# Performance work log

Hardware: AMD Instinct MI355X
Metric: run time of the kernel (lower is better)

Reference implementation:

```python
import jax, jax.numpy as jnp
import numpy as np

B, S, HID, MEM, NW = 32, 256, 1024, 256, 1024
PLAST, IMP = 0.1, 1.0
W_SCALE = 0.02  # sane init for projection weights


def setup_inputs() -> dict:
    key = jax.random.key(0)
    ks = jax.random.split(key, 24)
    n = lambda k, sh, s=1.0: jax.random.normal(k, sh, dtype=jnp.float32) * s
    inp = {
        "q": n(ks[0], (B, S, HID)),
        "data": n(ks[1], (NW, HID)),
        "episodic_k": n(ks[2], (MEM, HID)),
        "episodic_v": n(ks[3], (MEM, HID)),
        "semantic_k": n(ks[4], (MEM, HID)),
        "semantic_v": n(ks[5], (MEM, HID)),
        "working_m": n(ks[6], (1, 10, HID)),
    }
    i = 7
    for name in ("atte", "atts", "attw"):
        inp[name + "_in_w"] = n(ks[i], (3 * HID, HID), W_SCALE); i += 1
        inp[name + "_in_b"] = jnp.zeros((3 * HID,), jnp.float32)
        inp[name + "_out_w"] = n(ks[i], (HID, HID), W_SCALE); i += 1
        inp[name + "_out_b"] = jnp.zeros((HID,), jnp.float32)
    inp["proj_w"] = n(ks[i], (HID, 3 * HID), W_SCALE)
    inp["proj_b"] = jnp.zeros((HID,), jnp.float32)
    return inp


def mha_shared_kv(q, k, v, in_w, in_b, out_w, out_b, n_heads):
    # q: [B,S,H]; k,v: [M,H] (memory bank shared across the batch)
    d = q.shape[-1] // n_heads
    wq, wk, wv = jnp.split(in_w, 3, axis=0)
    bq, bk, bv = jnp.split(in_b, 3)
    Bq, Sq, _ = q.shape
    M = k.shape[0]
    qh = (q @ wq.T + bq).reshape(Bq, Sq, n_heads, d)   # [B,S,h,d]
    kh = (k @ wk.T + bk).reshape(M, n_heads, d)        # [M,h,d]
    vh = (v @ wv.T + bv).reshape(M, n_heads, d)
    scale = 1.0 / jnp.sqrt(jnp.float32(d))
    att = jax.nn.softmax(jnp.einsum('bshd,mhd->bhsm', qh, kh) * scale, axis=-1)
    o = jnp.einsum('bhsm,mhd->bshd', att, vh).reshape(Bq, Sq, -1)
    return o @ out_w.T + out_b


def reference(q, data, episodic_k, episodic_v, semantic_k, semantic_v, working_m,
              atte_in_w, atte_in_b, atte_out_w, atte_out_b,
              atts_in_w, atts_in_b, atts_out_w, atts_out_b,
              attw_in_w, attw_in_b, attw_out_w, attw_out_b,
              proj_w, proj_b):
    # ---- write(data, 'episodic'): softmax-addressed fast-weight update ----
    probs = jax.nn.softmax(data @ episodic_k.T, axis=-1)          # [N,M]
    w = probs * (PLAST * IMP)                                     # [N,M]
    u = w.mean(axis=0)[:, None]                                   # [M,1] mean update strength per slot
    writes = jnp.einsum('nm,nh->mh', w, data) / NW                # mean_n data[n]*w[n,m]
    ek = jax.lax.stop_gradient(episodic_k * (1.0 - u) + writes)   # .data assignment -> no grad
    ev = jax.lax.stop_gradient(episodic_v * (1.0 - u) + writes)
    # ---- read(q): 3 small attentions over memory banks, concat, project ----
    e_r = mha_shared_kv(q, ek, ev, atte_in_w, atte_in_b, atte_out_w, atte_out_b, 16)
    s_r = mha_shared_kv(q, semantic_k, semantic_v, atts_in_w, atts_in_b, atts_out_w, atts_out_b, 16)
    w_r = mha_shared_kv(q, working_m[0], working_m[0], attw_in_w, attw_in_b, attw_out_w, attw_out_b, 8)
    cat = jnp.concatenate((e_r, s_r, w_r), axis=-1)               # [B,S,3H]
    return cat @ proj_w.T + proj_b                                # [B,S,H]
```

## Files before the change

### kernel.cpp

```cpp
#include <hip/hip_runtime.h>
#include <hip/hip_bf16.h>


using bf = __hip_bfloat16;
using short8v = __attribute__((ext_vector_type(8))) short;
using f32x4  = __attribute__((ext_vector_type(4))) float;

#define GLOAD_LDS16(g, l) __builtin_amdgcn_global_load_lds( \
    (const __attribute__((address_space(1))) void*)(g), \
    (__attribute__((address_space(3))) void*)(l), 16, 0, 0)

__device__ inline float bf2f(unsigned short s) {
    union { unsigned u; float f; } c; c.u = ((unsigned)s) << 16; return c.f;
}
__device__ inline unsigned short f2bu(float x) {
    union { float f; unsigned u; } c; c.f = x;
    unsigned r = c.u + 0x7FFF + ((c.u >> 16) & 1);
    return (unsigned short)(r >> 16);
}
__device__ inline void storeC(float* p, float v) { *p = v; }
__device__ inline void storeC(bf* p, float v) { *p = __float2bfloat16(v); }

template <bool AF32>
__global__ __launch_bounds__(256) void gemm_bt(
    const void* __restrict__ Av, int lda,
    const bf* __restrict__ B, int ldb,
    float* __restrict__ part, int M, int N, int K)
{
    __shared__ short As[128 * 64];
    __shared__ short Bs[128 * 64];
    const int nbn = N >> 7;
    const int bm = blockIdx.x / nbn, bn = blockIdx.x % nbn;
    const int t = threadIdx.x;
    const int w = t >> 6, lane = t & 63;
    const int wr = w >> 1, wc = w & 1;
    const int l16 = lane & 15, lhi = lane >> 4;
    const int kc = K / gridDim.y;
    const int kbeg = blockIdx.y * kc, kend = kbeg + kc;

    f32x4 acc[4][4];
    #pragma unroll
    for (int i = 0; i < 4; ++i)
        #pragma unroll
        for (int j = 0; j < 4; ++j) { f32x4 z = {0.f, 0.f, 0.f, 0.f}; acc[i][j] = z; }

    const bf*    Arow  = (const bf*)Av + (size_t)bm * 128 * lda;
    const float* Afrow = (const float*)Av + (size_t)bm * 128 * lda;
    const bf*    Brow  = B + (size_t)bn * 128 * ldb;

    for (int k0 = kbeg; k0 < kend; k0 += 64) {
        #pragma unroll
        for (int j = 0; j < 4; ++j) {
            int u = (w * 4 + j) * 64 + lane;
            int row = u >> 3, c8 = u & 7;
            int slot = c8 ^ (row & 7);
            GLOAD_LDS16(Brow + (size_t)row * ldb + k0 + slot * 8, &Bs[(w * 4 + j) * 512]);
            if (!AF32)
                GLOAD_LDS16(Arow + (size_t)row * lda + k0 + slot * 8, &As[(w * 4 + j) * 512]);
        }
        if (AF32) {
            #pragma unroll
            for (int r = 0; r < 4; ++r) {
                int u = t + (r << 8);
                int row = u >> 3, c8 = u & 7;
                const float* src = Afrow + (size_t)row * lda + k0 + c8 * 8;
                float4 v0 = *(const float4*)src;
                float4 v1 = *(const float4*)(src + 4);
                short8v sv;
                sv[0] = (short)f2bu(v0.x); sv[1] = (short)f2bu(v0.y);
                sv[2] = (short)f2bu(v0.z); sv[3] = (short)f2bu(v0.w);
                sv[4] = (short)f2bu(v1.x); sv[5] = (short)f2bu(v1.y);
                sv[6] = (short)f2bu(v1.z); sv[7] = (short)f2bu(v1.w);
                *(short8v*)&As[row * 64 + ((c8 ^ (row & 7)) * 8)] = sv;
            }
        }
        __syncthreads();
        #pragma unroll
        for (int kk = 0; kk < 2; ++kk) {
            short8v af[4], bfr[4];
            #pragma unroll
            for (int mt = 0; mt < 4; ++mt) {
                int row = wr * 64 + mt * 16 + l16;
                int slot = (kk * 4 + lhi) ^ (row & 7);
                af[mt] = *(const short8v*)&As[row * 64 + slot * 8];
            }
            #pragma unroll
            for (int nt = 0; nt < 4; ++nt) {
                int row = wc * 64 + nt * 16 + l16;
                int slot = (kk * 4 + lhi) ^ (row & 7);
                bfr[nt] = *(const short8v*)&Bs[row * 64 + slot * 8];
            }
            #pragma unroll
            for (int mt = 0; mt < 4; ++mt)
                #pragma unroll
                for (int nt = 0; nt < 4; ++nt)
                    acc[mt][nt] = __builtin_amdgcn_mfma_f32_16x16x32_bf16(
                        af[mt], bfr[nt], acc[mt][nt], 0, 0, 0);
        }
        __syncthreads();
    }
    #pragma unroll
    for (int mt = 0; mt < 4; ++mt)
        #pragma unroll
        for (int nt = 0; nt < 4; ++nt) {
            int col = bn * 128 + wc * 64 + nt * 16 + l16;
            #pragma unroll
            for (int j = 0; j < 4; ++j) {
                int rowg = bm * 128 + wr * 64 + mt * 16 + lhi * 4 + j;
                part[(size_t)blockIdx.y * M * N + (size_t)rowg * N + col] = acc[mt][nt][j];
            }
        }
}

template <typename CT, bool AF32, bool XSWZ>
__global__ __launch_bounds__(512) void gemm256(
    const void* __restrict__ Av, int lda,
    const bf* __restrict__ B, int ldb,
    const float* __restrict__ bias,
    CT* __restrict__ C, int ldc,
    int M, int N, int K)
{
    __shared__ short As[256 * 64];
    __shared__ short Bs[128 * 64];
    const int nbn = N >> 7;
    int bid = blockIdx.x;
    if (XSWZ) bid = (bid & 7) * (gridDim.x >> 3) + (bid >> 3);
    const int bm = bid / nbn, bn = bid % nbn;
    const int t = threadIdx.x;
    const int w = t >> 6, lane = t & 63;
    const int wr = w >> 1, wc = w & 1;
    const int l16 = lane & 15, lhi = lane >> 4;

    f32x4 acc[4][4];
    #pragma unroll
    for (int i = 0; i < 4; ++i)
        #pragma unroll
        for (int j = 0; j < 4; ++j) { f32x4 z = {0.f, 0.f, 0.f, 0.f}; acc[i][j] = z; }

    const bf*    Arow  = (const bf*)Av + (size_t)bm * 256 * lda;
    const float* Afrow = (const float*)Av + (size_t)bm * 256 * lda;
    const bf*    Brow  = B + (size_t)bn * 128 * ldb;

    for (int k0 = 0; k0 < K; k0 += 64) {
        #pragma unroll
        for (int j = 0; j < 2; ++j) {
            int u = t + (j << 9);
            int row = u >> 3, c8 = u & 7;
            int slot = c8 ^ (row & 7);
            GLOAD_LDS16(Brow + (size_t)row * ldb + k0 + slot * 8, &Bs[(j * 8 + w) * 512]);
        }
        if (!AF32) {
            #pragma unroll
            for (int j = 0; j < 4; ++j) {
                int u = t + (j << 9);
                int row = u >> 3, c8 = u & 7;
                int slot = c8 ^ (row & 7);
                GLOAD_LDS16(Arow + (size_t)row * lda + k0 + slot * 8, &As[(j * 8 + w) * 512]);
            }
        } else {
            #pragma unroll
            for (int r = 0; r < 4; ++r) {
                int u = t + (r << 9);
                int row = u >> 3, c8 = u & 7;
                const float* src = Afrow + (size_t)row * lda + k0 + c8 * 8;
                float4 v0 = *(const float4*)src;
                float4 v1 = *(const float4*)(src + 4);
                short8v sv;
                sv[0] = (short)f2bu(v0.x); sv[1] = (short)f2bu(v0.y);
                sv[2] = (short)f2bu(v0.z); sv[3] = (short)f2bu(v0.w);
                sv[4] = (short)f2bu(v1.x); sv[5] = (short)f2bu(v1.y);
                sv[6] = (short)f2bu(v1.z); sv[7] = (short)f2bu(v1.w);
                *(short8v*)&As[row * 64 + ((c8 ^ (row & 7)) * 8)] = sv;
            }
        }
        __syncthreads();
        #pragma unroll
        for (int kk = 0; kk < 2; ++kk) {
            short8v af[4], bfr[4];
            #pragma unroll
            for (int mt = 0; mt < 4; ++mt) {
                int row = wr * 64 + mt * 16 + l16;
                int slot = (kk * 4 + lhi) ^ (row & 7);
                af[mt] = *(const short8v*)&As[row * 64 + slot * 8];
            }
            #pragma unroll
            for (int nt = 0; nt < 4; ++nt) {
                int row = wc * 64 + nt * 16 + l16;
                int slot = (kk * 4 + lhi) ^ (row & 7);
                bfr[nt] = *(const short8v*)&Bs[row * 64 + slot * 8];
            }
            #pragma unroll
            for (int mt = 0; mt < 4; ++mt)
                #pragma unroll
                for (int nt = 0; nt < 4; ++nt)
                    acc[mt][nt] = __builtin_amdgcn_mfma_f32_16x16x32_bf16(
                        af[mt], bfr[nt], acc[mt][nt], 0, 0, 0);
        }
        __syncthreads();
    }
    #pragma unroll
    for (int mt = 0; mt < 4; ++mt)
        #pragma unroll
        for (int nt = 0; nt < 4; ++nt) {
            int col = bn * 128 + wc * 64 + nt * 16 + l16;
            float bv = bias ? bias[col] : 0.0f;
            #pragma unroll
            for (int j = 0; j < 4; ++j) {
                int rowg = bm * 256 + wr * 64 + mt * 16 + lhi * 4 + j;
                storeC(&C[(size_t)rowg * ldc + col], acc[mt][nt][j] + bv);
            }
        }
}

struct GG { const float* A; const bf* B; const float* bias; bf* out;
            int lda, ldb, M, N, ldo, xoff; };
struct GG7 { GG g[7]; };

__global__ __launch_bounds__(256) void ggemm(GG7 P)
{
    __shared__ short As[128 * 64];
    __shared__ short Bs[128 * 64];
    const int bid = blockIdx.x;
    int gidx = 0;
    #pragma unroll
    for (int i = 1; i < 7; ++i) if (bid >= P.g[i].xoff) gidx = i;
    const GG d = P.g[gidx];
    const int lb = bid - d.xoff;
    const int nbn = d.N >> 7;
    const int bm = lb / nbn, bn = lb % nbn;
    const int t = threadIdx.x;
    const int w = t >> 6, lane = t & 63;
    const int wr = w >> 1, wc = w & 1;
    const int l16 = lane & 15, lhi = lane >> 4;

    f32x4 acc[4][4];
    #pragma unroll
    for (int i = 0; i < 4; ++i)
        #pragma unroll
        for (int j = 0; j < 4; ++j) { f32x4 z = {0.f, 0.f, 0.f, 0.f}; acc[i][j] = z; }

    const float* Afrow = d.A + (size_t)bm * 128 * d.lda;
    const bf*    Brow  = d.B + (size_t)bn * 128 * d.ldb;

    for (int k0 = 0; k0 < 1024; k0 += 64) {
        #pragma unroll
        for (int j = 0; j < 4; ++j) {
            int u = (w * 4 + j) * 64 + lane;
            int row = u >> 3, c8 = u & 7;
            int slot = c8 ^ (row & 7);
            GLOAD_LDS16(Brow + (size_t)row * d.ldb + k0 + slot * 8, &Bs[(w * 4 + j) * 512]);
        }
        #pragma unroll
        for (int r = 0; r < 4; ++r) {
            int u = t + (r << 8);
            int row = u >> 3, c8 = u & 7;
            const float* src = Afrow + (size_t)row * d.lda + k0 + c8 * 8;
            float4 v0 = *(const float4*)src;
            float4 v1 = *(const float4*)(src + 4);
            short8v sv;
            sv[0] = (short)f2bu(v0.x); sv[1] = (short)f2bu(v0.y);
            sv[2] = (short)f2bu(v0.z); sv[3] = (short)f2bu(v0.w);
            sv[4] = (short)f2bu(v1.x); sv[5] = (short)f2bu(v1.y);
            sv[6] = (short)f2bu(v1.z); sv[7] = (short)f2bu(v1.w);
            *(short8v*)&As[row * 64 + ((c8 ^ (row & 7)) * 8)] = sv;
        }
        __syncthreads();
        #pragma unroll
        for (int kk = 0; kk < 2; ++kk) {
            short8v af[4], bfr[4];
            #pragma unroll
            for (int mt = 0; mt < 4; ++mt) {
                int row = wr * 64 + mt * 16 + l16;
                int slot = (kk * 4 + lhi) ^ (row & 7);
                af[mt] = *(const short8v*)&As[row * 64 + slot * 8];
            }
            #pragma unroll
            for (int nt = 0; nt < 4; ++nt) {
                int row = wc * 64 + nt * 16 + l16;
                int slot = (kk * 4 + lhi) ^ (row & 7);
                bfr[nt] = *(const short8v*)&Bs[row * 64 + slot * 8];
            }
            #pragma unroll
            for (int mt = 0; mt < 4; ++mt)
                #pragma unroll
                for (int nt = 0; nt < 4; ++nt)
                    acc[mt][nt] = __builtin_amdgcn_mfma_f32_16x16x32_bf16(
                        af[mt], bfr[nt], acc[mt][nt], 0, 0, 0);
        }
        __syncthreads();
    }
    #pragma unroll
    for (int mt = 0; mt < 4; ++mt)
        #pragma unroll
        for (int nt = 0; nt < 4; ++nt) {
            int col = bn * 128 + wc * 64 + nt * 16 + l16;
            float bv = d.bias ? d.bias[col] : 0.0f;
            #pragma unroll
            for (int j = 0; j < 4; ++j) {
                int rowg = bm * 128 + wr * 64 + mt * 16 + lhi * 4 + j;
                d.out[(size_t)rowg * d.ldo + col]
                    = __float2bfloat16(acc[mt][nt][j] + bv);
            }
        }
}

__global__ __launch_bounds__(512) void attn_es(
    bf* Ocat, const bf* __restrict__ khE, const bf* __restrict__ khS,
    const bf* __restrict__ vTE, const bf* __restrict__ vTS)
{
    __shared__ short Ks[256 * 64];
    __shared__ short Vs[64 * 256];
    const int bank = blockIdx.x >> 10;
    const int lbid = blockIdx.x & 1023;
    const bf* kh  = bank ? khS : khE;
    const bf* vhT = bank ? vTS : vTE;
    bf* QO = Ocat + bank * 1024;
    const int qt = lbid >> 4, head = lbid & 15;
    const int t = threadIdx.x, w = t >> 6, lane = t & 63;
    const int l16 = lane & 15, lhi = lane >> 4;
    const float scale = 0.125f;

    #pragma unroll
    for (int j = 0; j < 4; ++j) {
        int ublk = w * 4 + j;
        int u = ublk * 64 + lane;
        { int row = u >> 3, c8 = u & 7;
          int slot = c8 ^ (row & 7);
          GLOAD_LDS16(kh + (size_t)row * 1024 + head * 64 + slot * 8, &Ks[ublk * 512]); }
        { int row = u >> 5, c16 = u & 31;
          int slot = c16 ^ (row & 7);
          GLOAD_LDS16(vhT + (size_t)(head * 64 + row) * 256 + slot * 8, &Vs[ublk * 512]); }
    }
    const int qr = qt * 128 + w * 16 + l16;
    short8v aq0 = *(const short8v*)(QO + (size_t)qr * 3072 + head * 64 + lhi * 8);
    short8v aq1 = *(const short8v*)(QO + (size_t)qr * 3072 + head * 64 + 32 + lhi * 8);
    __syncthreads();

    f32x4 sc[16];
    #pragma unroll
    for (int nt = 0; nt < 16; ++nt) { f32x4 z = {0.f, 0.f, 0.f, 0.f}; sc[nt] = z; }
    #pragma unroll
    for (int nt = 0; nt < 16; ++nt) {
        int row = nt * 16 + l16;
        #pragma unroll
        for (int kk = 0; kk < 2; ++kk) {
            int slot = (kk * 4 + lhi) ^ (row & 7);
            short8v b = *(const short8v*)&Ks[row * 64 + slot * 8];
            sc[nt] = __builtin_amdgcn_mfma_f32_16x16x32_bf16(kk ? aq1 : aq0, b, sc[nt], 0, 0, 0);
        }
    }
    float inv[4];
    #pragma unroll
    for (int j = 0; j < 4; ++j) {
        float m_ = -1e30f;
        #pragma unroll
        for (int nt = 0; nt < 16; ++nt) m_ = fmaxf(m_, sc[nt][j]);
        #pragma unroll
        for (int off = 8; off; off >>= 1) m_ = fmaxf(m_, __shfl_xor(m_, off));
        float s_ = 0.f;
        #pragma unroll
        for (int nt = 0; nt < 16; ++nt) {
            float e = __expf((sc[nt][j] - m_) * scale);
            sc[nt][j] = e; s_ += e;
        }
        #pragma unroll
        for (int off = 8; off; off >>= 1) s_ += __shfl_xor(s_, off);
        inv[j] = 1.0f / s_;
    }
    __syncthreads();

    char* Pw = (char*)Ks + w * 4096;
    f32x4 oa[4];
    #pragma unroll
    for (int nt = 0; nt < 4; ++nt) { f32x4 z = {0.f, 0.f, 0.f, 0.f}; oa[nt] = z; }
    #pragma unroll
    for (int h = 0; h < 2; ++h) {
        #pragma unroll
        for (int nt = 0; nt < 8; ++nt) {
            int colL = nt * 16 + l16;
            #pragma unroll
            for (int j = 0; j < 4; ++j) {
                int row = lhi * 4 + j;
                *(short*)(Pw + row * 256 + ((colL * 2) ^ ((row & 7) << 4)))
                    = (short)f2bu(sc[h * 8 + nt][j] * inv[j]);
            }
        }
        #pragma unroll
        for (int kk = 0; kk < 4; ++kk) {
            short8v a = *(const short8v*)(Pw + l16 * 256 + (((kk * 32 + lhi * 8) * 2) ^ ((l16 & 7) << 4)));
            #pragma unroll
            for (int nt = 0; nt < 4; ++nt) {
                int row = nt * 16 + l16;
                int m = h * 128 + kk * 32 + lhi * 8;
                short8v b = *(const short8v*)((const char*)Vs + row * 512 + ((m * 2) ^ ((row & 7) << 4)));
                oa[nt] = __builtin_amdgcn_mfma_f32_16x16x32_bf16(a, b, oa[nt], 0, 0, 0);
            }
        }
    }
    #pragma unroll
    for (int nt = 0; nt < 4; ++nt)
        #pragma unroll
        for (int j = 0; j < 4; ++j)
            QO[(size_t)(qt * 128 + w * 16 + lhi * 4 + j) * 3072 + head * 64 + nt * 16 + l16]
                = __float2bfloat16(oa[nt][j]);
}

__global__ __launch_bounds__(256) void attn_w(
    bf* QOp, const bf* __restrict__ khw, const bf* __restrict__ vhw)
{
    const int bs = blockIdx.x;
    const int t = threadIdx.x;
    const int head = t >> 5;
    const int dg = head * 128 + (t & 31) * 4;

    ushort4 qv = *(const ushort4*)(QOp + (size_t)bs * 3072 + dg);
    float q0 = bf2f(qv.x), q1 = bf2f(qv.y), q2 = bf2f(qv.z), q3 = bf2f(qv.w);
    float s[10];
    #pragma unroll
    for (int m = 0; m < 10; ++m) {
        ushort4 kv = *(const ushort4*)(khw + (size_t)m * 1024 + dg);
        float pr = q0 * bf2f(kv.x) + q1 * bf2f(kv.y) + q2 * bf2f(kv.z) + q3 * bf2f(kv.w);
        #pragma unroll
        for (int off = 16; off; off >>= 1) pr += __shfl_xor(pr, off);
        s[m] = pr * 0.08838834764831845f;
    }
    float mx = s[0];
    #pragma unroll
    for (int m = 1; m < 10; ++m) mx = fmaxf(mx, s[m]);
    float pp[10], sum = 0.f;
    #pragma unroll
    for (int m = 0; m < 10; ++m) { pp[m] = __expf(s[m] - mx); sum += pp[m]; }
    float inv = 1.0f / sum;
    float o0 = 0, o1 = 0, o2 = 0, o3 = 0;
    #pragma unroll
    for (int m = 0; m < 10; ++m) {
        ushort4 vv = *(const ushort4*)(vhw + (size_t)m * 1024 + dg);
        o0 += pp[m] * bf2f(vv.x); o1 += pp[m] * bf2f(vv.y);
        o2 += pp[m] * bf2f(vv.z); o3 += pp[m] * bf2f(vv.w);
    }
    bf* op = QOp + (size_t)bs * 3072 + dg;
    op[0] = __float2bfloat16(o0 * inv); op[1] = __float2bfloat16(o1 * inv);
    op[2] = __float2bfloat16(o2 * inv); op[3] = __float2bfloat16(o3 * inv);
}

struct CS { const float* src; bf* dst; int voff; };
struct MP {
    CS cs[8];
    const float* tsrc[4]; bf* tdst[4];
    const float* ow[3]; const float* ob[3]; const float* ib[3];
    float* bp;
    const float* inb_e; const float* inb_s; float* bqcat3;
    const float* wm; const float* inw_w; const float* inb_w;
    bf* khw; bf* vhw;
};

__global__ __launch_bounds__(256) void megaprep(MP P)
{
    __shared__ unsigned short tile[64][65];
    const int bid = blockIdx.x;
    const int t = threadIdx.x;
    if (bid < 13824) {
        int gi = bid * 256 + t;
        int gidx = 0;
        #pragma unroll
        for (int i = 1; i < 8; ++i) if (gi >= P.cs[i].voff) gidx = i;
        int i = (gi - P.cs[gidx].voff) * 4;
        float4 v = *(const float4*)(P.cs[gidx].src + i);
        ushort4 o;
        o.x = f2bu(v.x); o.y = f2bu(v.y); o.z = f2bu(v.z); o.w = f2bu(v.w);
        *(ushort4*)((unsigned short*)P.cs[gidx].dst + i) = o;
    } else if (bid < 14848) {
        int lb = bid - 13824;
        int sel = lb >> 8, bb = lb & 255;
        const float* in = P.tsrc[sel];
        bf* outT = P.tdst[sel];
        int bx = bb & 15, by = bb >> 4;
        int r0 = by * 64, c0 = bx * 64;
        int tr = t >> 4, tc4 = (t & 15) * 4;
        #pragma unroll
        for (int i = 0; i < 4; ++i) {
            int r = tr + i * 16;
            float4 v = *(const float4*)(in + (size_t)(r0 + r) * 1024 + c0 + tc4);
            tile[r][tc4 + 0] = f2bu(v.x); tile[r][tc4 + 1] = f2bu(v.y);
            tile[r][tc4 + 2] = f2bu(v.z); tile[r][tc4 + 3] = f2bu(v.w);
        }
        __syncthreads();
        #pragma unroll
        for (int i = 0; i < 4; ++i) {
            int r = tr + i * 16;
            ushort4 v;
            v.x = tile[tc4 + 0][r]; v.y = tile[tc4 + 1][r];
            v.z = tile[tc4 + 2][r]; v.w = tile[tc4 + 3][r];
            *(ushort4*)((unsigned short*)outT + (size_t)(c0 + r) * 1024 + r0 + tc4) = v;
        }
    } else if (bid < 15616) {
        int g = (bid - 14848) * 4 + (t >> 6);
        int lane = t & 63;
        int bank = g >> 10, j = g & 1023;
        const float* ow = P.ow[bank];
        const float* xx = P.ib[bank] + 2048;
        const float* wrow = ow + (size_t)j * 1024;
        float acc = 0.f;
        #pragma unroll
        for (int cc = 0; cc < 4; ++cc) {
            float4 a = *(const float4*)(wrow + lane * 16 + cc * 4);
            float4 x = *(const float4*)(xx + lane * 16 + cc * 4);
            acc += a.x * x.x + a.y * x.y + a.z * x.z + a.w * x.w;
        }
        #pragma unroll
        for (int off = 32; off; off >>= 1) acc += __shfl_xor(acc, off);
        if (lane == 0) P.bp[g] = acc + P.ob[bank][j];
    } else if (bid < 15628) {
        int i = (bid - 15616) * 256 + t;
        if (i < 1024) P.bqcat3[i] = P.inb_e[i];
        else if (i < 2048) P.bqcat3[i] = P.inb_s[i - 1024];
        else P.bqcat3[i] = P.inb_w[i - 2048];
    } else {
        int o = (bid - 15628) * 4 + (t >> 6);
        int lane = t & 63;
        int sel = o >= 10240;
        int o2 = o - sel * 10240;
        int m = o2 >> 10, c = o2 & 1023;
        const float* wrow = P.inw_w + (size_t)(1024 + sel * 1024 + c) * 1024;
        const float* xrow = P.wm + (size_t)m * 1024;
        float acc = 0.f;
        #pragma unroll
        for (int cc = 0; cc < 4; ++cc) {
            float4 a = *(const float4*)(wrow + lane * 16 + cc * 4);
            float4 x = *(const float4*)(xrow + lane * 16 + cc * 4);
            acc += a.x * x.x + a.y * x.y + a.z * x.z + a.w * x.w;
        }
        #pragma unroll
        for (int off = 32; off; off >>= 1) acc += __shfl_xor(acc, off);
        if (lane == 0) {
            float v = acc + (sel ? 0.f : P.inb_w[1024 + c]);
            (sel ? P.vhw : P.khw)[(size_t)m * 1024 + c] = __float2bfloat16(v);
        }
    }
}


__global__ __launch_bounds__(256) void btot_kern(
    const float* __restrict__ bp, const float* __restrict__ pw,
    const float* __restrict__ pb, float* __restrict__ btot)
{
    int j = blockIdx.x * 4 + (threadIdx.x >> 6);
    int lane = threadIdx.x & 63;
    const float* row = pw + (size_t)j * 3072;
    float acc = 0.f;
    #pragma unroll
    for (int it = 0; it < 12; ++it) {
        int c = lane * 4 + it * 256;
        float4 a = *(const float4*)(row + c);
        float4 x = *(const float4*)(bp + c);
        acc += a.x * x.x + a.y * x.y + a.z * x.z + a.w * x.w;
    }
    #pragma unroll
    for (int off = 32; off; off >>= 1) acc += __shfl_xor(acc, off);
    if (lane == 0) btot[j] = acc + pb[j];
}

__global__ __launch_bounds__(256) void write_softmax_p(const float* __restrict__ part,
                                                       bf* __restrict__ wT)
{
    const int n = blockIdx.x, m = threadIdx.x;
    float s = 0.f;
    #pragma unroll
    for (int k = 0; k < 8; ++k) s += part[(size_t)k * 262144 + n * 256 + m];
    float mx = s;
    #pragma unroll
    for (int off = 32; off; off >>= 1) mx = fmaxf(mx, __shfl_xor(mx, off));
    __shared__ float red[4], red2[4];
    int w = threadIdx.x >> 6;
    if ((threadIdx.x & 63) == 0) red[w] = mx;
    __syncthreads();
    mx = fmaxf(fmaxf(red[0], red[1]), fmaxf(red[2], red[3]));
    float e = __expf(s - mx);
    float sm = e;
    #pragma unroll
    for (int off = 32; off; off >>= 1) sm += __shfl_xor(sm, off);
    if ((threadIdx.x & 63) == 0) red2[w] = sm;
    __syncthreads();
    sm = red2[0] + red2[1] + red2[2] + red2[3];
    wT[(size_t)m * 1024 + n] = __float2bfloat16(0.1f * e / sm);
}

__global__ __launch_bounds__(256) void usum_kern(const bf* __restrict__ wT, float* __restrict__ u)
{
    int w = threadIdx.x >> 6, lane = threadIdx.x & 63;
    int m = blockIdx.x * 4 + w;
    const bf* row = wT + (size_t)m * 1024;
    float s = 0.f;
    for (int i = lane; i < 1024; i += 64) s += __bfloat162float(row[i]);
    #pragma unroll
    for (int off = 32; off; off >>= 1) s += __shfl_xor(s, off);
    if (lane == 0) u[m] = s * (1.0f / 1024.0f);
}

__global__ __launch_bounds__(256) void update_fused(
    const float* __restrict__ epk, const float* __restrict__ epv,
    const float* __restrict__ u, const float* __restrict__ part,
    float* __restrict__ ekf, bf* __restrict__ evb)
{
    int i = blockIdx.x * 256 + threadIdx.x;
    int m = i >> 10;
    float wr = 0.f;
    #pragma unroll
    for (int k = 0; k < 8; ++k) wr += part[(size_t)k * 262144 + i];
    wr *= (1.0f / 1024.0f);
    float f = 1.0f - u[m];
    ekf[i] = epk[i] * f + wr;
    evb[i] = __float2bfloat16(epv[i] * f + wr);
}

extern "C" void kernel_launch(void* const* d_in, const int* in_sizes, int n_in,
                              void* d_out, int out_size, void* d_ws, size_t ws_size,
                              hipStream_t stream)
{
    const float* q     = (const float*)d_in[0];
    const float* data  = (const float*)d_in[1];
    const float* epk   = (const float*)d_in[2];
    const float* epv   = (const float*)d_in[3];
    const float* smk   = (const float*)d_in[4];
    const float* smv   = (const float*)d_in[5];
    const float* wm    = (const float*)d_in[6];
    const float* inw_e = (const float*)d_in[7];  const float* inb_e = (const float*)d_in[8];
    const float* ow_e  = (const float*)d_in[9];  const float* ob_e  = (const float*)d_in[10];
    const float* inw_s = (const float*)d_in[11]; const float* inb_s = (const float*)d_in[12];
    const float* ow_s  = (const float*)d_in[13]; const float* ob_s  = (const float*)d_in[14];
    const float* inw_w = (const float*)d_in[15]; const float* inb_w = (const float*)d_in[16];
    const float* ow_w  = (const float*)d_in[17]; const float* ob_w  = (const float*)d_in[18];
    const float* pw    = (const float*)d_in[19]; const float* pb    = (const float*)d_in[20];
    float* out  = (float*)d_out;
    float* part = (float*)d_out;
    bf* qb = (bf*)((char*)d_out + 8388608);

    char* p = (char*)d_ws;
    auto alloc = [&](size_t bytes) -> char* {
        char* r = p; p += (bytes + 255) & ~(size_t)255; return r;
    };
    float* u      = (float*)alloc(256 * 4);
    float* bp     = (float*)alloc(3072 * 4);
    float* btot   = (float*)alloc(1024 * 4);
    float* bqcat3 = (float*)alloc(3072 * 4);
    float* ekf    = (float*)alloc((size_t)256 * 1024 * 4);
    bf* wT     = (bf*)alloc(256 * 1024 * 2);
    bf* dT     = (bf*)alloc((size_t)1024 * 1024 * 2);
    bf* epkb   = (bf*)alloc(256 * 1024 * 2);
    bf* smvb   = (bf*)alloc(256 * 1024 * 2);
    bf* evb    = (bf*)alloc(256 * 1024 * 2);
    bf* khE    = (bf*)alloc(256 * 1024 * 2);
    bf* khS    = (bf*)alloc(256 * 1024 * 2);
    bf* vTE    = (bf*)alloc((size_t)1024 * 256 * 2);
    bf* vTS    = (bf*)alloc((size_t)1024 * 256 * 2);
    bf* khw    = (bf*)alloc(10 * 1024 * 2);
    bf* vhw    = (bf*)alloc(10 * 1024 * 2);
    bf* Wall   = (bf*)alloc((size_t)3072 * 1024 * 2);
    bf* WkE    = (bf*)alloc((size_t)1024 * 1024 * 2);
    bf* WkS    = (bf*)alloc((size_t)1024 * 1024 * 2);
    bf* owT0   = (bf*)alloc((size_t)1024 * 1024 * 2);
    bf* owT1   = (bf*)alloc((size_t)1024 * 1024 * 2);
    bf* owT2   = (bf*)alloc((size_t)1024 * 1024 * 2);
    bf* Gcat   = (bf*)alloc((size_t)1024 * 3072 * 2);
    bf* Ocat   = (bf*)alloc((size_t)8192 * 3072 * 2);
    if ((size_t)(p - (char*)d_ws) > ws_size) return;

    {
        MP P;
        CS cs[8] = { {q, qb, 0},
                     {epk, epkb, 2097152}, {smv, smvb, 2162688},
                     {inw_e, Wall, 2228224},
                     {inw_s, Wall + (size_t)1024 * 1024, 2490368},
                     {inw_w, Wall + (size_t)2048 * 1024, 2752512},
                     {inw_e + (size_t)1024 * 1024, WkE, 3014656},
                     {inw_s + (size_t)1024 * 1024, WkS, 3276800} };
        for (int i = 0; i < 8; ++i) P.cs[i] = cs[i];
        P.tsrc[0] = data; P.tdst[0] = dT;
        P.tsrc[1] = ow_e; P.tdst[1] = owT0;
        P.tsrc[2] = ow_s; P.tdst[2] = owT1;
        P.tsrc[3] = ow_w; P.tdst[3] = owT2;
        P.ow[0] = ow_e; P.ow[1] = ow_s; P.ow[2] = ow_w;
        P.ob[0] = ob_e; P.ob[1] = ob_s; P.ob[2] = ob_w;
        P.ib[0] = inb_e; P.ib[1] = inb_s; P.ib[2] = inb_w;
        P.bp = bp;
        P.inb_e = inb_e; P.inb_s = inb_s; P.bqcat3 = bqcat3;
        P.wm = wm; P.inw_w = inw_w; P.inb_w = inb_w;
        P.khw = khw; P.vhw = vhw;
        megaprep<<<20748, 256, 0, stream>>>(P);
    }
    btot_kern<<<256, 256, 0, stream>>>(bp, pw, pb, btot);

    gemm_bt<true><<<dim3(16, 8), 256, 0, stream>>>(data, 1024, epkb, 1024, part, 1024, 256, 1024);
    write_softmax_p<<<1024, 256, 0, stream>>>(part, wT);
    usum_kern<<<64, 256, 0, stream>>>(wT, u);
    gemm_bt<false><<<dim3(16, 8), 256, 0, stream>>>(wT, 1024, dT, 1024, part, 256, 1024, 1024);
    update_fused<<<1024, 256, 0, stream>>>(epk, epv, u, part, ekf, evb);

    gemm256<bf, false, true><<<768, 512, 0, stream>>>(
        qb, 1024, Wall, 1024, bqcat3, Ocat, 3072, 8192, 3072, 1024);

    {
        GG7 G = {{
            { ekf,                         WkE,  inb_e + 1024, khE,         1024, 1024,  256, 1024, 1024, 0   },
            { smk,                         WkS,  inb_s + 1024, khS,         1024, 1024,  256, 1024, 1024, 16  },
            { inw_e + (size_t)2048 * 1024, evb,  nullptr,      vTE,         1024, 1024, 1024,  256,  256, 32  },
            { inw_s + (size_t)2048 * 1024, smvb, nullptr,      vTS,         1024, 1024, 1024,  256,  256, 48  },
            { pw + 0,                      owT0, nullptr,      Gcat + 0,    3072, 1024, 1024, 1024, 3072, 64  },
            { pw + 1024,                   owT1, nullptr,      Gcat + 1024, 3072, 1024, 1024, 1024, 3072, 128 },
            { pw + 2048,                   owT2, nullptr,      Gcat + 2048, 3072, 1024, 1024, 1024, 3072, 192 },
        }};
        ggemm<<<256, 256, 0, stream>>>(G);
    }

    attn_es<<<2048, 512, 0, stream>>>(Ocat, khE, khS, vTE, vTS);
    attn_w<<<8192, 256, 0, stream>>>(Ocat + 2048, khw, vhw);

    gemm256<float, false, true><<<256, 512, 0, stream>>>(
        Ocat, 3072, Gcat, 3072, btot, out, 1024, 8192, 1024, 3072);
}
```

Before: 299.7 us.

## Pre-convert fp32 GEMM operands to bf16 and double-buffer the final projection GEMM

Moves the fp32-to-bf16 conversion of data, proj_w, semantic_k and the V input weights into the megaprep pass. The GEMM kernels can then load A tiles straight into LDS with async global-to-LDS loads instead of converting in registers. The episodic key update now writes bf16 directly. The final output GEMM switches to a new double-buffered kernel that overlaps the next K-tile load with MFMA compute. The cost is larger megaprep work, extra workspace, and a scratch bf16 proj_w copy placed in the output buffer.

```diff
diff --git a/kernel.cpp b/kernel.cpp
--- a/kernel.cpp
+++ b/kernel.cpp
@@ -21,9 +21,8 @@
 __device__ inline void storeC(float* p, float v) { *p = v; }
 __device__ inline void storeC(bf* p, float v) { *p = __float2bfloat16(v); }
 
-template <bool AF32>
 __global__ __launch_bounds__(256) void gemm_bt(
-    const void* __restrict__ Av, int lda,
+    const bf* __restrict__ A, int lda,
     const bf* __restrict__ B, int ldb,
     float* __restrict__ part, int M, int N, int K)
 {
@@ -44,9 +43,8 @@
         #pragma unroll
         for (int j = 0; j < 4; ++j) { f32x4 z = {0.f, 0.f, 0.f, 0.f}; acc[i][j] = z; }
 
-    const bf*    Arow  = (const bf*)Av + (size_t)bm * 128 * lda;
-    const float* Afrow = (const float*)Av + (size_t)bm * 128 * lda;
-    const bf*    Brow  = B + (size_t)bn * 128 * ldb;
+    const bf* Arow = A + (size_t)bm * 128 * lda;
+    const bf* Brow = B + (size_t)bn * 128 * ldb;
 
     for (int k0 = kbeg; k0 < kend; k0 += 64) {
         #pragma unroll
@@ -55,24 +53,7 @@
             int row = u >> 3, c8 = u & 7;
             int slot = c8 ^ (row & 7);
             GLOAD_LDS16(Brow + (size_t)row * ldb + k0 + slot * 8, &Bs[(w * 4 + j) * 512]);
-            if (!AF32)
-                GLOAD_LDS16(Arow + (size_t)row * lda + k0 + slot * 8, &As[(w * 4 + j) * 512]);
-        }
-        if (AF32) {
-            #pragma unroll
-            for (int r = 0; r < 4; ++r) {
-                int u = t + (r << 8);
-                int row = u >> 3, c8 = u & 7;
-                const float* src = Afrow + (size_t)row * lda + k0 + c8 * 8;
-                float4 v0 = *(const float4*)src;
-                float4 v1 = *(const float4*)(src + 4);
-                short8v sv;
-                sv[0] = (short)f2bu(v0.x); sv[1] = (short)f2bu(v0.y);
-                sv[2] = (short)f2bu(v0.z); sv[3] = (short)f2bu(v0.w);
-                sv[4] = (short)f2bu(v1.x); sv[5] = (short)f2bu(v1.y);
-                sv[6] = (short)f2bu(v1.z); sv[7] = (short)f2bu(v1.w);
-                *(short8v*)&As[row * 64 + ((c8 ^ (row & 7)) * 8)] = sv;
-            }
+            GLOAD_LDS16(Arow + (size_t)row * lda + k0 + slot * 8, &As[(w * 4 + j) * 512]);
         }
         __syncthreads();
         #pragma unroll
@@ -112,9 +93,9 @@
         }
 }
 
-template <typename CT, bool AF32, bool XSWZ>
+template <typename CT>
 __global__ __launch_bounds__(512) void gemm256(
-    const void* __restrict__ Av, int lda,
+    const bf* __restrict__ A, int lda,
     const bf* __restrict__ B, int ldb,
     const float* __restrict__ bias,
     CT* __restrict__ C, int ldc,
@@ -124,7 +105,7 @@
     __shared__ short Bs[128 * 64];
     const int nbn = N >> 7;
     int bid = blockIdx.x;
-    if (XSWZ) bid = (bid & 7) * (gridDim.x >> 3) + (bid >> 3);
+    bid = (bid & 7) * (gridDim.x >> 3) + (bid >> 3);
     const int bm = bid / nbn, bn = bid % nbn;
     const int t = threadIdx.x;
     const int w = t >> 6, lane = t & 63;
@@ -137,9 +118,8 @@
         #pragma unroll
         for (int j = 0; j < 4; ++j) { f32x4 z = {0.f, 0.f, 0.f, 0.f}; acc[i][j] = z; }
 
-    const bf*    Arow  = (const bf*)Av + (size_t)bm * 256 * lda;
-    const float* Afrow = (const float*)Av + (size_t)bm * 256 * lda;
-    const bf*    Brow  = B + (size_t)bn * 128 * ldb;
+    const bf* Arow = A + (size_t)bm * 256 * lda;
+    const bf* Brow = B + (size_t)bn * 128 * ldb;
 
     for (int k0 = 0; k0 < K; k0 += 64) {
         #pragma unroll
@@ -149,29 +129,12 @@
             int slot = c8 ^ (row & 7);
             GLOAD_LDS16(Brow + (size_t)row * ldb + k0 + slot * 8, &Bs[(j * 8 + w) * 512]);
         }
-        if (!AF32) {
-            #pragma unroll
-            for (int j = 0; j < 4; ++j) {
-                int u = t + (j << 9);
-                int row = u >> 3, c8 = u & 7;
-                int slot = c8 ^ (row & 7);
-                GLOAD_LDS16(Arow + (size_t)row * lda + k0 + slot * 8, &As[(j * 8 + w) * 512]);
-            }
-        } else {
-            #pragma unroll
-            for (int r = 0; r < 4; ++r) {
-                int u = t + (r << 9);
-                int row = u >> 3, c8 = u & 7;
-                const float* src = Afrow + (size_t)row * lda + k0 + c8 * 8;
-                float4 v0 = *(const float4*)src;
-                float4 v1 = *(const float4*)(src + 4);
-                short8v sv;
-                sv[0] = (short)f2bu(v0.x); sv[1] = (short)f2bu(v0.y);
-                sv[2] = (short)f2bu(v0.z); sv[3] = (short)f2bu(v0.w);
-                sv[4] = (short)f2bu(v1.x); sv[5] = (short)f2bu(v1.y);
-                sv[6] = (short)f2bu(v1.z); sv[7] = (short)f2bu(v1.w);
-                *(short8v*)&As[row * 64 + ((c8 ^ (row & 7)) * 8)] = sv;
-            }
+        #pragma unroll
+        for (int j = 0; j < 4; ++j) {
+            int u = t + (j << 9);
+            int row = u >> 3, c8 = u & 7;
+            int slot = c8 ^ (row & 7);
+            GLOAD_LDS16(Arow + (size_t)row * lda + k0 + slot * 8, &As[(j * 8 + w) * 512]);
         }
         __syncthreads();
         #pragma unroll
@@ -212,7 +175,119 @@
         }
 }
 
-struct GG { const float* A; const bf* B; const float* bias; bf* out;
+__global__ __launch_bounds__(512) void gemm256db(
+    const bf* __restrict__ A, int lda,
+    const bf* __restrict__ B, int ldb,
+    const float* __restrict__ bias,
+    float* __restrict__ C, int ldc,
+    int M, int N, int K)
+{
+    __shared__ short As0[256 * 64];
+    __shared__ short Bs0[128 * 64];
+    __shared__ short As1[256 * 64];
+    __shared__ short Bs1[128 * 64];
+    const int nbn = N >> 7;
+    int bid = blockIdx.x;
+    bid = (bid & 7) * (gridDim.x >> 3) + (bid >> 3);
+    const int bm = bid / nbn, bn = bid % nbn;
+    const int t = threadIdx.x;
+    const int w = t >> 6, lane = t & 63;
+    const int wr = w >> 1, wc = w & 1;
+    const int l16 = lane & 15, lhi = lane >> 4;
+
+    f32x4 acc[4][4];
+    #pragma unroll
+    for (int i = 0; i < 4; ++i)
+        #pragma unroll
+        for (int j = 0; j < 4; ++j) { f32x4 z = {0.f, 0.f, 0.f, 0.f}; acc[i][j] = z; }
+
+    const bf* Arow = A + (size_t)bm * 256 * lda;
+    const bf* Brow = B + (size_t)bn * 128 * ldb;
+
+    auto stage = [&](short* Asd, short* Bsd, int k0) {
+        #pragma unroll
+        for (int j = 0; j < 2; ++j) {
+            int u = t + (j << 9);
+            int row = u >> 3, c8 = u & 7;
+            int slot = c8 ^ (row & 7);
+            GLOAD_LDS16(Brow + (size_t)row * ldb + k0 + slot * 8, &Bsd[(j * 8 + w) * 512]);
+        }
+        #pragma unroll
+        for (int j = 0; j < 4; ++j) {
+            int u = t + (j << 9);
+            int row = u >> 3, c8 = u & 7;
+            int slot = c8 ^ (row & 7);
+            GLOAD_LDS16(Arow + (size_t)row * lda + k0 + slot * 8, &Asd[(j * 8 + w) * 512]);
+        }
+    };
+    auto compute = [&](const short* Ass, const short* Bss) {
+        #pragma unroll
+        for (int kk = 0; kk < 2; ++kk) {
+            short8v af[4], bfr[4];
+            #pragma unroll
+            for (int mt = 0; mt < 4; ++mt) {
+                int row = wr * 64 + mt * 16 + l16;
+                int slot = (kk * 4 + lhi) ^ (row & 7);
+                af[mt] = *(const short8v*)&Ass[row * 64 + slot * 8];
+            }
+            #pragma unroll
+            for (int nt = 0; nt < 4; ++nt) {
+                int row = wc * 64 + nt * 16 + l16;
+                int slot = (kk * 4 + lhi) ^ (row & 7);
+                bfr[nt] = *(const short8v*)&Bss[row * 64 + slot * 8];
+            }
+            #pragma unroll
+            for (int mt = 0; mt < 4; ++mt)
+                #pragma unroll
+                for (int nt = 0; nt < 4; ++nt)
+                    acc[mt][nt] = __builtin_amdgcn_mfma_f32_16x16x32_bf16(
+                        af[mt], bfr[nt], acc[mt][nt], 0, 0, 0);
+        }
+    };
+
+    const int nt_ = K >> 6;
+    stage(As0, Bs0, 0);
+    stage(As1, Bs1, 64);
+    asm volatile("s_waitcnt vmcnt(6)" ::: "memory");
+    __builtin_amdgcn_sched_barrier(0);
+    __builtin_amdgcn_s_barrier();
+
+    for (int ti = 0; ti < nt_ - 2; ti += 2) {
+        compute(As0, Bs0);
+        __builtin_amdgcn_s_barrier();
+        stage(As0, Bs0, (ti + 2) << 6);
+        asm volatile("s_waitcnt vmcnt(6)" ::: "memory");
+        __builtin_amdgcn_sched_barrier(0);
+        __builtin_amdgcn_s_barrier();
+        compute(As1, Bs1);
+        __builtin_amdgcn_s_barrier();
+        stage(As1, Bs1, (ti + 3) << 6);
+        asm volatile("s_waitcnt vmcnt(6)" ::: "memory");
+        __builtin_amdgcn_sched_barrier(0);
+        __builtin_amdgcn_s_barrier();
+    }
+    compute(As0, Bs0);
+    __builtin_amdgcn_s_barrier();
+    asm volatile("s_waitcnt vmcnt(0)" ::: "memory");
+    __builtin_amdgcn_sched_barrier(0);
+    __builtin_amdgcn_s_barrier();
+    compute(As1, Bs1);
+
+    #pragma unroll
+    for (int mt = 0; mt < 4; ++mt)
+        #pragma unroll
+        for (int nt = 0; nt < 4; ++nt) {
+            int col = bn * 128 + wc * 64 + nt * 16 + l16;
+            float bv = bias ? bias[col] : 0.0f;
+            #pragma unroll
+            for (int j = 0; j < 4; ++j) {
+                int rowg = bm * 256 + wr * 64 + mt * 16 + lhi * 4 + j;
+                C[(size_t)rowg * ldc + col] = acc[mt][nt][j] + bv;
+            }
+        }
+}
+
+struct GG { const bf* A; const bf* B; const float* bias; bf* out;
             int lda, ldb, M, N, ldo, xoff; };
 struct GG7 { GG g[7]; };
 
@@ -239,8 +314,8 @@
         #pragma unroll
         for (int j = 0; j < 4; ++j) { f32x4 z = {0.f, 0.f, 0.f, 0.f}; acc[i][j] = z; }
 
-    const float* Afrow = d.A + (size_t)bm * 128 * d.lda;
-    const bf*    Brow  = d.B + (size_t)bn * 128 * d.ldb;
+    const bf* Afrow = d.A + (size_t)bm * 128 * d.lda;
+    const bf* Brow  = d.B + (size_t)bn * 128 * d.ldb;
 
     for (int k0 = 0; k0 < 1024; k0 += 64) {
         #pragma unroll
@@ -249,20 +324,7 @@
             int row = u >> 3, c8 = u & 7;
             int slot = c8 ^ (row & 7);
             GLOAD_LDS16(Brow + (size_t)row * d.ldb + k0 + slot * 8, &Bs[(w * 4 + j) * 512]);
-        }
-        #pragma unroll
-        for (int r = 0; r < 4; ++r) {
-            int u = t + (r << 8);
-            int row = u >> 3, c8 = u & 7;
-            const float* src = Afrow + (size_t)row * d.lda + k0 + c8 * 8;
-            float4 v0 = *(const float4*)src;
-            float4 v1 = *(const float4*)(src + 4);
-            short8v sv;
-            sv[0] = (short)f2bu(v0.x); sv[1] = (short)f2bu(v0.y);
-            sv[2] = (short)f2bu(v0.z); sv[3] = (short)f2bu(v0.w);
-            sv[4] = (short)f2bu(v1.x); sv[5] = (short)f2bu(v1.y);
-            sv[6] = (short)f2bu(v1.z); sv[7] = (short)f2bu(v1.w);
-            *(short8v*)&As[row * 64 + ((c8 ^ (row & 7)) * 8)] = sv;
+            GLOAD_LDS16(Afrow + (size_t)row * d.lda + k0 + slot * 8, &As[(w * 4 + j) * 512]);
         }
         __syncthreads();
         #pragma unroll
@@ -445,7 +507,7 @@
 
 struct CS { const float* src; bf* dst; int voff; };
 struct MP {
-    CS cs[8];
+    CS cs[13];
     const float* tsrc[4]; bf* tdst[4];
     const float* ow[3]; const float* ob[3]; const float* ib[3];
     float* bp;
@@ -459,18 +521,18 @@
     __shared__ unsigned short tile[64][65];
     const int bid = blockIdx.x;
     const int t = threadIdx.x;
-    if (bid < 13824) {
+    if (bid < 20224) {
         int gi = bid * 256 + t;
         int gidx = 0;
         #pragma unroll
-        for (int i = 1; i < 8; ++i) if (gi >= P.cs[i].voff) gidx = i;
+        for (int i = 1; i < 13; ++i) if (gi >= P.cs[i].voff) gidx = i;
         int i = (gi - P.cs[gidx].voff) * 4;
         float4 v = *(const float4*)(P.cs[gidx].src + i);
         ushort4 o;
         o.x = f2bu(v.x); o.y = f2bu(v.y); o.z = f2bu(v.z); o.w = f2bu(v.w);
         *(ushort4*)((unsigned short*)P.cs[gidx].dst + i) = o;
-    } else if (bid < 14848) {
-        int lb = bid - 13824;
+    } else if (bid < 21248) {
+        int lb = bid - 20224;
         int sel = lb >> 8, bb = lb & 255;
         const float* in = P.tsrc[sel];
         bf* outT = P.tdst[sel];
@@ -493,8 +555,8 @@
             v.z = tile[tc4 + 2][r]; v.w = tile[tc4 + 3][r];
             *(ushort4*)((unsigned short*)outT + (size_t)(c0 + r) * 1024 + r0 + tc4) = v;
         }
-    } else if (bid < 15616) {
-        int g = (bid - 14848) * 4 + (t >> 6);
+    } else if (bid < 22016) {
+        int g = (bid - 21248) * 4 + (t >> 6);
         int lane = t & 63;
         int bank = g >> 10, j = g & 1023;
         const float* ow = P.ow[bank];
@@ -510,13 +572,13 @@
         #pragma unroll
         for (int off = 32; off; off >>= 1) acc += __shfl_xor(acc, off);
         if (lane == 0) P.bp[g] = acc + P.ob[bank][j];
-    } else if (bid < 15628) {
-        int i = (bid - 15616) * 256 + t;
+    } else if (bid < 22028) {
+        int i = (bid - 22016) * 256 + t;
         if (i < 1024) P.bqcat3[i] = P.inb_e[i];
         else if (i < 2048) P.bqcat3[i] = P.inb_s[i - 1024];
         else P.bqcat3[i] = P.inb_w[i - 2048];
     } else {
-        int o = (bid - 15628) * 4 + (t >> 6);
+        int o = (bid - 22028) * 4 + (t >> 6);
         int lane = t & 63;
         int sel = o >= 10240;
         int o2 = o - sel * 10240;
@@ -600,7 +662,7 @@
 __global__ __launch_bounds__(256) void update_fused(
     const float* __restrict__ epk, const float* __restrict__ epv,
     const float* __restrict__ u, const float* __restrict__ part,
-    float* __restrict__ ekf, bf* __restrict__ evb)
+    bf* __restrict__ ekb, bf* __restrict__ evb)
 {
     int i = blockIdx.x * 256 + threadIdx.x;
     int m = i >> 10;
@@ -609,7 +671,7 @@
     for (int k = 0; k < 8; ++k) wr += part[(size_t)k * 262144 + i];
     wr *= (1.0f / 1024.0f);
     float f = 1.0f - u[m];
-    ekf[i] = epk[i] * f + wr;
+    ekb[i] = __float2bfloat16(epk[i] * f + wr);
     evb[i] = __float2bfloat16(epv[i] * f + wr);
 }
 
@@ -633,7 +695,8 @@
     const float* pw    = (const float*)d_in[19]; const float* pb    = (const float*)d_in[20];
     float* out  = (float*)d_out;
     float* part = (float*)d_out;
-    bf* qb = (bf*)((char*)d_out + 8388608);
+    bf* qb  = (bf*)((char*)d_out + 8388608);
+    bf* pwb = (bf*)((char*)d_out + 25165824);
 
     char* p = (char*)d_ws;
     auto alloc = [&](size_t bytes) -> char* {
@@ -643,11 +706,13 @@
     float* bp     = (float*)alloc(3072 * 4);
     float* btot   = (float*)alloc(1024 * 4);
     float* bqcat3 = (float*)alloc(3072 * 4);
-    float* ekf    = (float*)alloc((size_t)256 * 1024 * 4);
     bf* wT     = (bf*)alloc(256 * 1024 * 2);
     bf* dT     = (bf*)alloc((size_t)1024 * 1024 * 2);
+    bf* datab  = (bf*)alloc((size_t)1024 * 1024 * 2);
     bf* epkb   = (bf*)alloc(256 * 1024 * 2);
+    bf* smkb   = (bf*)alloc(256 * 1024 * 2);
     bf* smvb   = (bf*)alloc(256 * 1024 * 2);
+    bf* ekb    = (bf*)alloc(256 * 1024 * 2);
     bf* evb    = (bf*)alloc(256 * 1024 * 2);
     bf* khE    = (bf*)alloc(256 * 1024 * 2);
     bf* khS    = (bf*)alloc(256 * 1024 * 2);
@@ -658,6 +723,8 @@
     bf* Wall   = (bf*)alloc((size_t)3072 * 1024 * 2);
     bf* WkE    = (bf*)alloc((size_t)1024 * 1024 * 2);
     bf* WkS    = (bf*)alloc((size_t)1024 * 1024 * 2);
+    bf* WvE    = (bf*)alloc((size_t)1024 * 1024 * 2);
+    bf* WvS    = (bf*)alloc((size_t)1024 * 1024 * 2);
     bf* owT0   = (bf*)alloc((size_t)1024 * 1024 * 2);
     bf* owT1   = (bf*)alloc((size_t)1024 * 1024 * 2);
     bf* owT2   = (bf*)alloc((size_t)1024 * 1024 * 2);
@@ -667,14 +734,19 @@
 
     {
         MP P;
-        CS cs[8] = { {q, qb, 0},
-                     {epk, epkb, 2097152}, {smv, smvb, 2162688},
-                     {inw_e, Wall, 2228224},
-                     {inw_s, Wall + (size_t)1024 * 1024, 2490368},
-                     {inw_w, Wall + (size_t)2048 * 1024, 2752512},
-                     {inw_e + (size_t)1024 * 1024, WkE, 3014656},
-                     {inw_s + (size_t)1024 * 1024, WkS, 3276800} };
-        for (int i = 0; i < 8; ++i) P.cs[i] = cs[i];
+        CS cs[13] = { {q, qb, 0},
+                      {epk,  epkb, 2097152}, {smv, smvb, 2162688},
+                      {inw_e, Wall, 2228224},
+                      {inw_s, Wall + (size_t)1024 * 1024, 2490368},
+                      {inw_w, Wall + (size_t)2048 * 1024, 2752512},
+                      {inw_e + (size_t)1024 * 1024, WkE, 3014656},
+                      {inw_s + (size_t)1024 * 1024, WkS, 3276800},
+                      {data, datab, 3538944},
+                      {pw, pwb, 3801088},
+                      {smk, smkb, 4587520},
+                      {inw_e + (size_t)2048 * 1024, WvE, 4653056},
+                      {inw_s + (size_t)2048 * 1024, WvS, 4915200} };
+        for (int i = 0; i < 13; ++i) P.cs[i] = cs[i];
         P.tsrc[0] = data; P.tdst[0] = dT;
         P.tsrc[1] = ow_e; P.tdst[1] = owT0;
         P.tsrc[2] = ow_s; P.tdst[2] = owT1;
@@ -686,28 +758,28 @@
         P.inb_e = inb_e; P.inb_s = inb_s; P.bqcat3 = bqcat3;
         P.wm = wm; P.inw_w = inw_w; P.inb_w = inb_w;
         P.khw = khw; P.vhw = vhw;
-        megaprep<<<20748, 256, 0, stream>>>(P);
+        megaprep<<<27148, 256, 0, stream>>>(P);
     }
     btot_kern<<<256, 256, 0, stream>>>(bp, pw, pb, btot);
 
-    gemm_bt<true><<<dim3(16, 8), 256, 0, stream>>>(data, 1024, epkb, 1024, part, 1024, 256, 1024);
+    gemm_bt<<<dim3(16, 8), 256, 0, stream>>>(datab, 1024, epkb, 1024, part, 1024, 256, 1024);
     write_softmax_p<<<1024, 256, 0, stream>>>(part, wT);
     usum_kern<<<64, 256, 0, stream>>>(wT, u);
-    gemm_bt<false><<<dim3(16, 8), 256, 0, stream>>>(wT, 1024, dT, 1024, part, 256, 1024, 1024);
-    update_fused<<<1024, 256, 0, stream>>>(epk, epv, u, part, ekf, evb);
-
-    gemm256<bf, false, true><<<768, 512, 0, stream>>>(
+    gemm_bt<<<dim3(16, 8), 256, 0, stream>>>(wT, 1024, dT, 1024, part, 256, 1024, 1024);
+    update_fused<<<1024, 256, 0, stream>>>(epk, epv, u, part, ekb, evb);
+
+    gemm256<bf><<<768, 512, 0, stream>>>(
         qb, 1024, Wall, 1024, bqcat3, Ocat, 3072, 8192, 3072, 1024);
 
     {
         GG7 G = {{
-            { ekf,                         WkE,  inb_e + 1024, khE,         1024, 1024,  256, 1024, 1024, 0   },
-            { smk,                         WkS,  inb_s + 1024, khS,         1024, 1024,  256, 1024, 1024, 16  },
-            { inw_e + (size_t)2048 * 1024, evb,  nullptr,      vTE,         1024, 1024, 1024,  256,  256, 32  },
-            { inw_s + (size_t)2048 * 1024, smvb, nullptr,      vTS,         1024, 1024, 1024,  256,  256, 48  },
-            { pw + 0,                      owT0, nullptr,      Gcat + 0,    3072, 1024, 1024, 1024, 3072, 64  },
-            { pw + 1024,                   owT1, nullptr,      Gcat + 1024, 3072, 1024, 1024, 1024, 3072, 128 },
-            { pw + 2048,                   owT2, nullptr,      Gcat + 2048, 3072, 1024, 1024, 1024, 3072, 192 },
+            { ekb,        WkE,  inb_e + 1024, khE,         1024, 1024,  256, 1024, 1024, 0   },
+            { smkb,       WkS,  inb_s + 1024, khS,         1024, 1024,  256, 1024, 1024, 16  },
+            { WvE,        evb,  nullptr,      vTE,         1024, 1024, 1024,  256,  256, 32  },
+            { WvS,        smvb, nullptr,      vTS,         1024, 1024, 1024,  256,  256, 48  },
+            { pwb + 0,    owT0, nullptr,      Gcat + 0,    3072, 1024, 1024, 1024, 3072, 64  },
+            { pwb + 1024, owT1, nullptr,      Gcat + 1024, 3072, 1024, 1024, 1024, 3072, 128 },
+            { pwb + 2048, owT2, nullptr,      Gcat + 2048, 3072, 1024, 1024, 1024, 3072, 192 },
         }};
         ggemm<<<256, 256, 0, stream>>>(G);
     }
@@ -715,6 +787,6 @@
     attn_es<<<2048, 512, 0, stream>>>(Ocat, khE, khS, vTE, vTS);
     attn_w<<<8192, 256, 0, stream>>>(Ocat + 2048, khw, vhw);
 
-    gemm256<float, false, true><<<256, 512, 0, stream>>>(
+    gemm256db<<<256, 512, 0, stream>>>(
         Ocat, 3072, Gcat, 3072, btot, out, 1024, 8192, 1024, 3072);
 }
```

After: 277.4 us. 1.08x faster.
